# Optimization experiments

Hardware: AMD Instinct MI355X
Metric: run time of the kernel (lower is better)

Reference implementation:

```python
import jax, jax.numpy as jnp
import numpy as np

N, K, D = 8192, 4096, 256


def setup_inputs() -> dict:
    key = jax.random.key(0)
    kx, kc, kw = jax.random.split(key, 3)
    x = jax.random.normal(kx, (N, D), dtype=jnp.float32)
    centers = jax.random.normal(kc, (K, D), dtype=jnp.float32)
    w = jax.random.normal(kw, (K,), dtype=jnp.float32)
    # bandwidth chosen so exp(-sigma * d2) stays in a healthy range for
    # Gaussian data where E[||x-c||^2] ~= 2*D
    sigma = jnp.asarray(1.0 / (2.0 * D), dtype=jnp.float32)
    return {"x": x, "centers": centers, "w": w, "sigma": sigma}


def reference(x, centers, w, sigma):
    # phi[n,k] = exp(-sigma * ||x_n - c_k||^2), computed via the GEMM
    x2 = jnp.sum(x * x, axis=-1, keepdims=True)          # [N,1]
    c2 = jnp.sum(centers * centers, axis=-1)             # [K]
    d2 = x2 + c2 - 2.0 * jnp.einsum('nd,kd->nk', x, centers)  # [N,K]
    d2 = jnp.maximum(d2, 0.0)  # clamp tiny negative round-off
    phi = jnp.exp(-sigma * d2)                           # [N,K]
    # (w * phi).sum(1) == phi @ w
    return jnp.einsum('nk,k->n', phi, w)                 # [N]
```

## Files before the change

kernel.cpp:

```cpp
#include <hip/hip_runtime.h>

#define NROWS 8192
#define NCENT 4096
#define DIM   256

#define AS1 __attribute__((address_space(1)))
#define AS3 __attribute__((address_space(3)))

typedef short bf16x8 __attribute__((ext_vector_type(8)));
typedef float f32x4  __attribute__((ext_vector_type(4)));

__device__ inline unsigned short f2bf(float f) {
    unsigned u = __float_as_uint(f);
    return (unsigned short)((u + 0x7fffu + ((u >> 16) & 1u)) >> 16);
}

__global__ __launch_bounds__(256) void prep_kernel(const float* __restrict__ x,
                                                   const float* __restrict__ c,
                                                   float* __restrict__ norms,
                                                   unsigned short* __restrict__ xbf,
                                                   unsigned short* __restrict__ cbf) {
    const int t = threadIdx.x, lane = t & 63;
    const int wbase = (blockIdx.x * 4 + (t >> 6)) * 4;
    #pragma unroll
    for (int rr = 0; rr < 4; ++rr) {
        const int gw = wbase + rr;
        const float* src;
        unsigned short* dst;
        if (gw < NROWS) { src = x + (size_t)gw * DIM;           dst = xbf + (size_t)gw * DIM; }
        else            { src = c + (size_t)(gw - NROWS) * DIM; dst = cbf + (size_t)(gw - NROWS) * DIM; }
        float4 v = ((const float4*)src)[lane];
        ushort4 b;
        b.x = f2bf(v.x); b.y = f2bf(v.y); b.z = f2bf(v.z); b.w = f2bf(v.w);
        ((ushort4*)dst)[lane] = b;
        float s = v.x * v.x + v.y * v.y + v.z * v.z + v.w * v.w;
        #pragma unroll
        for (int m = 32; m; m >>= 1) s += __shfl_xor(s, m);
        if (lane == 0) norms[gw] = s;
    }
}

__global__ __launch_bounds__(256) void rbf_mfma(const unsigned short* __restrict__ xbf,
                                                const unsigned short* __restrict__ cbf,
                                                const float* __restrict__ w,
                                                const float* __restrict__ sigp,
                                                const float* __restrict__ norms,
                                                float* __restrict__ out) {
    __shared__ __align__(16) short As[128 * 32];
    __shared__ __align__(16) short Bs[128 * 32];

    const int t    = threadIdx.x;
    const int wave = t >> 6, lane = t & 63;
    const int m0   = blockIdx.y * 128;
    const int n0   = blockIdx.x * 128;
    const int wy   = wave >> 1, wx = wave & 1;
    const int lr   = lane & 15;
    const int g    = lane >> 4;

    const int r_in = lane >> 2;
    const int c_l  = (lane & 3) ^ ((r_in >> 1) & 3);
    const unsigned short* ga0 = xbf + (size_t)(m0 + 32 * wave + r_in) * DIM + c_l * 8;
    const unsigned short* ga1 = ga0 + 16 * DIM;
    const unsigned short* gb0 = cbf + (size_t)(n0 + 32 * wave + r_in) * DIM + c_l * 8;
    const unsigned short* gb1 = gb0 + 16 * DIM;
    short* la0 = As + (32 * wave) * 32;
    short* la1 = la0 + 16 * 32;
    short* lb0 = Bs + (32 * wave) * 32;
    short* lb1 = lb0 + 16 * 32;

    int aoff[4], boff[4];
    #pragma unroll
    for (int i = 0; i < 4; ++i) {
        int r = 64 * wy + 16 * i + lr;
        aoff[i] = r * 32 + ((g ^ ((r >> 1) & 3)) * 8);
    }
    #pragma unroll
    for (int j = 0; j < 4; ++j) {
        int r = 64 * wx + 16 * j + lr;
        boff[j] = r * 32 + ((g ^ ((r >> 1) & 3)) * 8);
    }

    f32x4 acc[4][4];
    #pragma unroll
    for (int i = 0; i < 4; ++i)
        #pragma unroll
        for (int j = 0; j < 4; ++j) acc[i][j] = f32x4{0, 0, 0, 0};

    #pragma unroll
    for (int kk = 0; kk < DIM / 32; ++kk) {
        __syncthreads();
        const int ko = kk * 32;
        __builtin_amdgcn_global_load_lds((const AS1 void*)(ga0 + ko), (AS3 void*)la0, 16, 0, 0);
        __builtin_amdgcn_global_load_lds((const AS1 void*)(ga1 + ko), (AS3 void*)la1, 16, 0, 0);
        __builtin_amdgcn_global_load_lds((const AS1 void*)(gb0 + ko), (AS3 void*)lb0, 16, 0, 0);
        __builtin_amdgcn_global_load_lds((const AS1 void*)(gb1 + ko), (AS3 void*)lb1, 16, 0, 0);
        __syncthreads();

        bf16x8 a[4], b[4];
        #pragma unroll
        for (int i = 0; i < 4; ++i) a[i] = *(const bf16x8*)(As + aoff[i]);
        #pragma unroll
        for (int j = 0; j < 4; ++j) b[j] = *(const bf16x8*)(Bs + boff[j]);
        #pragma unroll
        for (int i = 0; i < 4; ++i)
            #pragma unroll
            for (int j = 0; j < 4; ++j)
                acc[i][j] = __builtin_amdgcn_mfma_f32_16x16x32_bf16(a[i], b[j], acc[i][j], 0, 0, 0);
    }

    const float sigma = sigp[0];
    const float* x2 = norms;
    const float* c2 = norms + NROWS;

    float c2v[4], wv[4];
    #pragma unroll
    for (int j = 0; j < 4; ++j) {
        int n = n0 + 64 * wx + 16 * j + lr;
        c2v[j] = c2[n];
        wv[j]  = w[n];
    }

    #pragma unroll
    for (int i = 0; i < 4; ++i) {
        const int mbase = m0 + 64 * wy + 16 * i + 4 * g;
        float4 x2v = *(const float4*)(x2 + mbase);
        float rs[4] = {0.f, 0.f, 0.f, 0.f};
        #pragma unroll
        for (int j = 0; j < 4; ++j) {
            #pragma unroll
            for (int r = 0; r < 4; ++r) {
                float x2r = (r == 0) ? x2v.x : (r == 1) ? x2v.y : (r == 2) ? x2v.z : x2v.w;
                float d2 = x2r + c2v[j] - 2.0f * acc[i][j][r];
                d2 = fmaxf(d2, 0.0f);
                rs[r] += wv[j] * __expf(-sigma * d2);
            }
        }
        #pragma unroll
        for (int r = 0; r < 4; ++r) {
            rs[r] += __shfl_xor(rs[r], 1);
            rs[r] += __shfl_xor(rs[r], 2);
            rs[r] += __shfl_xor(rs[r], 4);
            rs[r] += __shfl_xor(rs[r], 8);
        }
        if (lr == 0) {
            #pragma unroll
            for (int r = 0; r < 4; ++r) atomicAdd(&out[mbase + r], rs[r]);
        }
    }
}

__global__ __launch_bounds__(256) void norms_kernel(const float* __restrict__ x,
                                                    const float* __restrict__ c,
                                                    float* __restrict__ ws) {
    int t = threadIdx.x, lane = t & 63;
    int gw = blockIdx.x * 4 + (t >> 6);
    const float* src;
    float* dst;
    if (gw < NROWS) { src = x + (size_t)gw * DIM;           dst = ws + gw; }
    else            { src = c + (size_t)(gw - NROWS) * DIM; dst = ws + gw; }
    float4 v = ((const float4*)src)[lane];
    float s = v.x * v.x + v.y * v.y + v.z * v.z + v.w * v.w;
    #pragma unroll
    for (int m = 32; m; m >>= 1) s += __shfl_xor(s, m);
    if (lane == 0) *dst = s;
}

__global__ __launch_bounds__(256) void rbf_kernel(const float* __restrict__ x,
                                                  const float* __restrict__ cent,
                                                  const float* __restrict__ w,
                                                  const float* __restrict__ sigp,
                                                  const float* __restrict__ norms,
                                                  float* __restrict__ out) {
    __shared__ __align__(16) short xs[64 * 32];
    __shared__ __align__(16) short cs[64 * 32];
    const int t = threadIdx.x;
    const int m0 = blockIdx.y * 64, n0 = blockIdx.x * 64;
    const int srow = t >> 2, seg = t & 3;
    const int pchunk = seg ^ ((srow >> 1) & 3);
    const int sidx = srow * 32 + pchunk * 8;
    const float* xg = x    + (size_t)(m0 + srow) * DIM + seg * 8;
    const float* cg = cent + (size_t)(n0 + srow) * DIM + seg * 8;
    const int lane = t & 63, wave = t >> 6;
    const int lr = lane & 15, lg = lane >> 4;
    const int arow = 16 * wave + lr;
    const int aidx = arow * 32 + ((lg ^ ((arow >> 1) & 3)) * 8);
    f32x4 acc[4] = {f32x4{0,0,0,0}, f32x4{0,0,0,0}, f32x4{0,0,0,0}, f32x4{0,0,0,0}};
    for (int k0 = 0; k0 < DIM; k0 += 32) {
        float4 f0 = *(const float4*)(xg + k0);
        float4 f1 = *(const float4*)(xg + k0 + 4);
        float4 g0 = *(const float4*)(cg + k0);
        float4 g1 = *(const float4*)(cg + k0 + 4);
        __syncthreads();
        union { unsigned short s[8]; int4 v; } ux, uc;
        ux.s[0]=f2bf(f0.x); ux.s[1]=f2bf(f0.y); ux.s[2]=f2bf(f0.z); ux.s[3]=f2bf(f0.w);
        ux.s[4]=f2bf(f1.x); ux.s[5]=f2bf(f1.y); ux.s[6]=f2bf(f1.z); ux.s[7]=f2bf(f1.w);
        uc.s[0]=f2bf(g0.x); uc.s[1]=f2bf(g0.y); uc.s[2]=f2bf(g0.z); uc.s[3]=f2bf(g0.w);
        uc.s[4]=f2bf(g1.x); uc.s[5]=f2bf(g1.y); uc.s[6]=f2bf(g1.z); uc.s[7]=f2bf(g1.w);
        *(int4*)(xs + sidx) = ux.v;
        *(int4*)(cs + sidx) = uc.v;
        __syncthreads();
        bf16x8 a = *(const bf16x8*)(xs + aidx);
        #pragma unroll
        for (int bt = 0; bt < 4; ++bt) {
            const int brow = 16 * bt + lr;
            bf16x8 b = *(const bf16x8*)(cs + brow * 32 + ((lg ^ ((brow >> 1) & 3)) * 8));
            acc[bt] = __builtin_amdgcn_mfma_f32_16x16x32_bf16(a, b, acc[bt], 0, 0, 0);
        }
    }
    const float sigma = sigp[0];
    const float* x2 = norms;
    const float* c2 = norms + NROWS;
    const int rbase = m0 + 16 * wave + lg * 4;
    float x2v[4];
    #pragma unroll
    for (int r = 0; r < 4; ++r) x2v[r] = x2[rbase + r];
    float rs[4] = {0.f, 0.f, 0.f, 0.f};
    #pragma unroll
    for (int bt = 0; bt < 4; ++bt) {
        const int col = n0 + 16 * bt + lr;
        const float c2v = c2[col];
        const float wvv = w[col];
        #pragma unroll
        for (int r = 0; r < 4; ++r) {
            float d2 = x2v[r] + c2v - 2.0f * acc[bt][r];
            d2 = fmaxf(d2, 0.0f);
            rs[r] += wvv * __expf(-sigma * d2);
        }
    }
    #pragma unroll
    for (int r = 0; r < 4; ++r) {
        rs[r] += __shfl_xor(rs[r], 1);
        rs[r] += __shfl_xor(rs[r], 2);
        rs[r] += __shfl_xor(rs[r], 4);
        rs[r] += __shfl_xor(rs[r], 8);
    }
    if (lr == 0) {
        #pragma unroll
        for (int r = 0; r < 4; ++r) atomicAdd(&out[rbase + r], rs[r]);
    }
}

extern "C" void kernel_launch(void* const* d_in, const int* in_sizes, int n_in,
                              void* d_out, int out_size, void* d_ws, size_t ws_size,
                              hipStream_t stream) {
    const float* x    = (const float*)d_in[0];
    const float* cent = (const float*)d_in[1];
    const float* w    = (const float*)d_in[2];
    const float* sig  = (const float*)d_in[3];
    float* out = (float*)d_out;

    const size_t norms_elems = NROWS + NCENT;
    const size_t xbf_off  = norms_elems * sizeof(float);
    const size_t cbf_off  = xbf_off + (size_t)NROWS * DIM * sizeof(unsigned short);
    const size_t ws_need  = cbf_off + (size_t)NCENT * DIM * sizeof(unsigned short);

    hipMemsetAsync(d_out, 0, (size_t)out_size * sizeof(float), stream);

    if (ws_size >= ws_need) {
        float* norms = (float*)d_ws;
        unsigned short* xbf = (unsigned short*)((char*)d_ws + xbf_off);
        unsigned short* cbf = (unsigned short*)((char*)d_ws + cbf_off);
        prep_kernel<<<(NROWS + NCENT) / 16, 256, 0, stream>>>(x, cent, norms, xbf, cbf);
        rbf_mfma<<<dim3(NCENT / 128, NROWS / 128), 256, 0, stream>>>(xbf, cbf, w, sig, norms, out);
    } else {
        float* norms = (float*)d_ws;
        norms_kernel<<<(NROWS + NCENT) / 4, 256, 0, stream>>>(x, cent, norms);
        rbf_kernel<<<dim3(NCENT / 64, NROWS / 64), 256, 0, stream>>>(x, cent, w, sig, norms, out);
    }
}
```

Baseline: 104.8 us.

## Use 256x256 tiles with 8 waves, double-buffered LDS staging and block swizzle

The MFMA kernel moves from 128x128 tiles with 4 waves to 256x256 tiles with 8 waves, each wave computing a 128x64 sub-tile. Global-to-LDS loads now go into two buffers so the next K slice is fetched while the current one is multiplied, with manual vmcnt waits and barriers. A 1D grid with a block-index swizzle groups neighbouring tiles to improve L2 reuse. Each thread now holds twice the accumulators, which raises register pressure, and the grid shrinks to 512 blocks, which may limit occupancy.

Result: slower. 115.0 us (+9.7%).

```diff
diff --git a/kernel.cpp b/kernel.cpp
--- a/kernel.cpp
+++ b/kernel.cpp
@@ -40,22 +40,28 @@
     }
 }
 
-__global__ __launch_bounds__(256) void rbf_mfma(const unsigned short* __restrict__ xbf,
-                                                const unsigned short* __restrict__ cbf,
-                                                const float* __restrict__ w,
-                                                const float* __restrict__ sigp,
-                                                const float* __restrict__ norms,
-                                                float* __restrict__ out) {
-    __shared__ __align__(16) short As[128 * 32];
-    __shared__ __align__(16) short Bs[128 * 32];
+#define BUFS (256 * 32)
+
+__global__ __launch_bounds__(512, 2) void rbf_mfma256(const unsigned short* __restrict__ xbf,
+                                                      const unsigned short* __restrict__ cbf,
+                                                      const float* __restrict__ w,
+                                                      const float* __restrict__ sigp,
+                                                      const float* __restrict__ norms,
+                                                      float* __restrict__ out) {
+    __shared__ __align__(16) short As[2 * BUFS];
+    __shared__ __align__(16) short Bs[2 * BUFS];
 
     const int t    = threadIdx.x;
     const int wave = t >> 6, lane = t & 63;
-    const int m0   = blockIdx.y * 128;
-    const int n0   = blockIdx.x * 128;
-    const int wy   = wave >> 1, wx = wave & 1;
-    const int lr   = lane & 15;
-    const int g    = lane >> 4;
+
+    const int bid = blockIdx.x;
+    const int swz = (bid & 7) * 64 + (bid >> 3);
+    const int m0  = (swz >> 4) * 256;
+    const int n0  = (swz & 15) * 256;
+
+    const int wy = wave >> 2, wx = wave & 3;
+    const int lr = lane & 15;
+    const int g  = lane >> 4;
 
     const int r_in = lane >> 2;
     const int c_l  = (lane & 3) ^ ((r_in >> 1) & 3);
@@ -64,14 +70,24 @@
     const unsigned short* gb0 = cbf + (size_t)(n0 + 32 * wave + r_in) * DIM + c_l * 8;
     const unsigned short* gb1 = gb0 + 16 * DIM;
     short* la0 = As + (32 * wave) * 32;
-    short* la1 = la0 + 16 * 32;
     short* lb0 = Bs + (32 * wave) * 32;
-    short* lb1 = lb0 + 16 * 32;
-
-    int aoff[4], boff[4];
-    #pragma unroll
-    for (int i = 0; i < 4; ++i) {
-        int r = 64 * wy + 16 * i + lr;
+
+#define STAGE(buf, kk) do {                                                                             \
+        const int ko_ = (kk) * 32;                                                                      \
+        __builtin_amdgcn_global_load_lds((const AS1 void*)(ga0 + ko_),                                  \
+                                         (AS3 void*)(la0 + (buf) * BUFS), 16, 0, 0);                    \
+        __builtin_amdgcn_global_load_lds((const AS1 void*)(ga1 + ko_),                                  \
+                                         (AS3 void*)(la0 + (buf) * BUFS + 16 * 32), 16, 0, 0);          \
+        __builtin_amdgcn_global_load_lds((const AS1 void*)(gb0 + ko_),                                  \
+                                         (AS3 void*)(lb0 + (buf) * BUFS), 16, 0, 0);                    \
+        __builtin_amdgcn_global_load_lds((const AS1 void*)(gb1 + ko_),                                  \
+                                         (AS3 void*)(lb0 + (buf) * BUFS + 16 * 32), 16, 0, 0);          \
+    } while (0)
+
+    int aoff[8], boff[4];
+    #pragma unroll
+    for (int i = 0; i < 8; ++i) {
+        int r = 128 * wy + 16 * i + lr;
         aoff[i] = r * 32 + ((g ^ ((r >> 1) & 3)) * 8);
     }
     #pragma unroll
@@ -80,33 +96,43 @@
         boff[j] = r * 32 + ((g ^ ((r >> 1) & 3)) * 8);
     }
 
-    f32x4 acc[4][4];
-    #pragma unroll
-    for (int i = 0; i < 4; ++i)
+    f32x4 acc[8][4];
+    #pragma unroll
+    for (int i = 0; i < 8; ++i)
         #pragma unroll
         for (int j = 0; j < 4; ++j) acc[i][j] = f32x4{0, 0, 0, 0};
 
-    #pragma unroll
-    for (int kk = 0; kk < DIM / 32; ++kk) {
-        __syncthreads();
-        const int ko = kk * 32;
-        __builtin_amdgcn_global_load_lds((const AS1 void*)(ga0 + ko), (AS3 void*)la0, 16, 0, 0);
-        __builtin_amdgcn_global_load_lds((const AS1 void*)(ga1 + ko), (AS3 void*)la1, 16, 0, 0);
-        __builtin_amdgcn_global_load_lds((const AS1 void*)(gb0 + ko), (AS3 void*)lb0, 16, 0, 0);
-        __builtin_amdgcn_global_load_lds((const AS1 void*)(gb1 + ko), (AS3 void*)lb1, 16, 0, 0);
-        __syncthreads();
-
-        bf16x8 a[4], b[4];
-        #pragma unroll
-        for (int i = 0; i < 4; ++i) a[i] = *(const bf16x8*)(As + aoff[i]);
-        #pragma unroll
-        for (int j = 0; j < 4; ++j) b[j] = *(const bf16x8*)(Bs + boff[j]);
-        #pragma unroll
-        for (int i = 0; i < 4; ++i)
+    STAGE(0, 0);
+
+    #pragma unroll
+    for (int kk = 0; kk < 8; ++kk) {
+        const int cur = kk & 1;
+        if (kk < 7) {
+            STAGE(cur ^ 1, kk + 1);
+            asm volatile("s_waitcnt vmcnt(4)" ::: "memory");
+        } else {
+            asm volatile("s_waitcnt vmcnt(0)" ::: "memory");
+        }
+        __builtin_amdgcn_s_barrier();
+        __builtin_amdgcn_sched_barrier(0);
+
+        const short* Ab = As + cur * BUFS;
+        const short* Bb = Bs + cur * BUFS;
+        bf16x8 a[8], b[4];
+        #pragma unroll
+        for (int i = 0; i < 8; ++i) a[i] = *(const bf16x8*)(Ab + aoff[i]);
+        #pragma unroll
+        for (int j = 0; j < 4; ++j) b[j] = *(const bf16x8*)(Bb + boff[j]);
+        #pragma unroll
+        for (int i = 0; i < 8; ++i)
             #pragma unroll
             for (int j = 0; j < 4; ++j)
                 acc[i][j] = __builtin_amdgcn_mfma_f32_16x16x32_bf16(a[i], b[j], acc[i][j], 0, 0, 0);
-    }
+
+        __builtin_amdgcn_sched_barrier(0);
+        __builtin_amdgcn_s_barrier();
+    }
+#undef STAGE
 
     const float sigma = sigp[0];
     const float* x2 = norms;
@@ -121,8 +147,8 @@
     }
 
     #pragma unroll
-    for (int i = 0; i < 4; ++i) {
-        const int mbase = m0 + 64 * wy + 16 * i + 4 * g;
+    for (int i = 0; i < 8; ++i) {
+        const int mbase = m0 + 128 * wy + 16 * i + 4 * g;
         float4 x2v = *(const float4*)(x2 + mbase);
         float rs[4] = {0.f, 0.f, 0.f, 0.f};
         #pragma unroll
@@ -261,7 +287,7 @@
         unsigned short* xbf = (unsigned short*)((char*)d_ws + xbf_off);
         unsigned short* cbf = (unsigned short*)((char*)d_ws + cbf_off);
         prep_kernel<<<(NROWS + NCENT) / 16, 256, 0, stream>>>(x, cent, norms, xbf, cbf);
-        rbf_mfma<<<dim3(NCENT / 128, NROWS / 128), 256, 0, stream>>>(xbf, cbf, w, sig, norms, out);
+        rbf_mfma256<<<512, 512, 0, stream>>>(xbf, cbf, w, sig, norms, out);
     } else {
         float* norms = (float*)d_ws;
         norms_kernel<<<(NROWS + NCENT) / 4, 256, 0, stream>>>(x, cent, norms);
```

## Double-buffer LDS tiles in RBF GEMM and fold output zeroing into prep

Applied to the files above, without the earlier changes.

Double-buffers the LDS A/B tiles so the next K-slice's global-to-LDS loads are issued before the current slice's MFMAs, with one barrier per iteration instead of two. It also removes the hipMemsetAsync on the fast path and zeroes the output inside prep_kernel, saving one launch. In exchange, LDS use per block doubles, and correctness depends on the async LDS loads having finished by the time of the barrier.

After: 103.1 us (median of 2 runs). Within noise of the previous version (-1.7%).

```diff
diff --git a/kernel.cpp b/kernel.cpp
--- a/kernel.cpp
+++ b/kernel.cpp
@@ -19,8 +19,10 @@
                                                    const float* __restrict__ c,
                                                    float* __restrict__ norms,
                                                    unsigned short* __restrict__ xbf,
-                                                   unsigned short* __restrict__ cbf) {
+                                                   unsigned short* __restrict__ cbf,
+                                                   float* __restrict__ out) {
     const int t = threadIdx.x, lane = t & 63;
+    if (blockIdx.x < NROWS / 256) out[blockIdx.x * 256 + t] = 0.0f;
     const int wbase = (blockIdx.x * 4 + (t >> 6)) * 4;
     #pragma unroll
     for (int rr = 0; rr < 4; ++rr) {
@@ -40,14 +42,16 @@
     }
 }
 
+#define BUFH (128 * 32)
+
 __global__ __launch_bounds__(256) void rbf_mfma(const unsigned short* __restrict__ xbf,
                                                 const unsigned short* __restrict__ cbf,
                                                 const float* __restrict__ w,
                                                 const float* __restrict__ sigp,
                                                 const float* __restrict__ norms,
                                                 float* __restrict__ out) {
-    __shared__ __align__(16) short As[128 * 32];
-    __shared__ __align__(16) short Bs[128 * 32];
+    __shared__ __align__(16) short As[2 * BUFH];
+    __shared__ __align__(16) short Bs[2 * BUFH];
 
     const int t    = threadIdx.x;
     const int wave = t >> 6, lane = t & 63;
@@ -64,9 +68,19 @@
     const unsigned short* gb0 = cbf + (size_t)(n0 + 32 * wave + r_in) * DIM + c_l * 8;
     const unsigned short* gb1 = gb0 + 16 * DIM;
     short* la0 = As + (32 * wave) * 32;
-    short* la1 = la0 + 16 * 32;
     short* lb0 = Bs + (32 * wave) * 32;
-    short* lb1 = lb0 + 16 * 32;
+
+#define STAGE(buf, kk) do {                                                                  \
+        const int ko_ = (kk) * 32;                                                           \
+        __builtin_amdgcn_global_load_lds((const AS1 void*)(ga0 + ko_),                       \
+                                         (AS3 void*)(la0 + (buf) * BUFH), 16, 0, 0);         \
+        __builtin_amdgcn_global_load_lds((const AS1 void*)(ga1 + ko_),                       \
+                                         (AS3 void*)(la0 + (buf) * BUFH + 16 * 32), 16, 0, 0);\
+        __builtin_amdgcn_global_load_lds((const AS1 void*)(gb0 + ko_),                       \
+                                         (AS3 void*)(lb0 + (buf) * BUFH), 16, 0, 0);         \
+        __builtin_amdgcn_global_load_lds((const AS1 void*)(gb1 + ko_),                       \
+                                         (AS3 void*)(lb0 + (buf) * BUFH + 16 * 32), 16, 0, 0);\
+    } while (0)
 
     int aoff[4], boff[4];
     #pragma unroll
@@ -86,27 +100,30 @@
         #pragma unroll
         for (int j = 0; j < 4; ++j) acc[i][j] = f32x4{0, 0, 0, 0};
 
+    STAGE(0, 0);
+    __syncthreads();
+
     #pragma unroll
     for (int kk = 0; kk < DIM / 32; ++kk) {
-        __syncthreads();
-        const int ko = kk * 32;
-        __builtin_amdgcn_global_load_lds((const AS1 void*)(ga0 + ko), (AS3 void*)la0, 16, 0, 0);
-        __builtin_amdgcn_global_load_lds((const AS1 void*)(ga1 + ko), (AS3 void*)la1, 16, 0, 0);
-        __builtin_amdgcn_global_load_lds((const AS1 void*)(gb0 + ko), (AS3 void*)lb0, 16, 0, 0);
-        __builtin_amdgcn_global_load_lds((const AS1 void*)(gb1 + ko), (AS3 void*)lb1, 16, 0, 0);
-        __syncthreads();
-
+        const int cur = kk & 1;
+        if (kk < DIM / 32 - 1) STAGE(cur ^ 1, kk + 1);
+
+        const short* Ab = As + cur * BUFH;
+        const short* Bb = Bs + cur * BUFH;
         bf16x8 a[4], b[4];
         #pragma unroll
-        for (int i = 0; i < 4; ++i) a[i] = *(const bf16x8*)(As + aoff[i]);
-        #pragma unroll
-        for (int j = 0; j < 4; ++j) b[j] = *(const bf16x8*)(Bs + boff[j]);
+        for (int i = 0; i < 4; ++i) a[i] = *(const bf16x8*)(Ab + aoff[i]);
+        #pragma unroll
+        for (int j = 0; j < 4; ++j) b[j] = *(const bf16x8*)(Bb + boff[j]);
         #pragma unroll
         for (int i = 0; i < 4; ++i)
             #pragma unroll
             for (int j = 0; j < 4; ++j)
                 acc[i][j] = __builtin_amdgcn_mfma_f32_16x16x32_bf16(a[i], b[j], acc[i][j], 0, 0, 0);
-    }
+
+        __syncthreads();
+    }
+#undef STAGE
 
     const float sigma = sigp[0];
     const float* x2 = norms;
@@ -254,16 +271,15 @@
     const size_t cbf_off  = xbf_off + (size_t)NROWS * DIM * sizeof(unsigned short);
     const size_t ws_need  = cbf_off + (size_t)NCENT * DIM * sizeof(unsigned short);
 
-    hipMemsetAsync(d_out, 0, (size_t)out_size * sizeof(float), stream);
-
     if (ws_size >= ws_need) {
         float* norms = (float*)d_ws;
         unsigned short* xbf = (unsigned short*)((char*)d_ws + xbf_off);
         unsigned short* cbf = (unsigned short*)((char*)d_ws + cbf_off);
-        prep_kernel<<<(NROWS + NCENT) / 16, 256, 0, stream>>>(x, cent, norms, xbf, cbf);
+        prep_kernel<<<(NROWS + NCENT) / 16, 256, 0, stream>>>(x, cent, norms, xbf, cbf, out);
         rbf_mfma<<<dim3(NCENT / 128, NROWS / 128), 256, 0, stream>>>(xbf, cbf, w, sig, norms, out);
     } else {
         float* norms = (float*)d_ws;
+        hipMemsetAsync(d_out, 0, (size_t)out_size * sizeof(float), stream);
         norms_kernel<<<(NROWS + NCENT) / 4, 256, 0, stream>>>(x, cent, norms);
         rbf_kernel<<<dim3(NCENT / 64, NROWS / 64), 256, 0, stream>>>(x, cent, w, sig, norms, out);
     }
```
